# Kernel tuning notes

Hardware: AMD Instinct MI355X
Metric: run time of the kernel (lower is better)

Reference implementation:

```python
import jax, jax.numpy as jnp
import numpy as np

NEG_INF = jnp.finfo(jnp.float32).min


def setup_inputs() -> dict:
    key = jax.random.key(0)
    k1, k2, k3, k4 = jax.random.split(key, 4)
    B, T, C, H = 8, 2048, 1024, 128
    x = jax.random.normal(k1, (B, T, C), dtype=jnp.float32)
    # nn.Linear(n_embd, head_size, bias=False) -> weight [head_size, n_embd]
    s = 1.0 / np.sqrt(C)
    Wk = jax.random.normal(k2, (H, C), dtype=jnp.float32) * s
    Wq = jax.random.normal(k3, (H, C), dtype=jnp.float32) * s
    Wv = jax.random.normal(k4, (H, C), dtype=jnp.float32) * s
    return {"x": x, "Wk": Wk, "Wq": Wq, "Wv": Wv}


def reference(x, Wk, Wq, Wv):
    B, T, C = x.shape
    # projections: x [B,T,C] @ W.T [C,H] -> [B,T,H]
    k = jnp.einsum('btc,hc->bth', x, Wk)
    q = jnp.einsum('btc,hc->bth', x, Wq)
    v = jnp.einsum('btc,hc->bth', x, Wv)
    # NOTE: original scales by C**-0.5 (input channels), faithful here
    scores = jnp.einsum('bqh,bkh->bqk', q, k) * (C ** -0.5)
    causal = jnp.tril(jnp.ones((T, T), dtype=bool))  # tril[:T,:T]
    scores = jnp.where(causal, scores, NEG_INF)
    attn = jax.nn.softmax(scores, axis=-1)
    # dropout(p=0.1) is identity in eval mode; omitted for deterministic reference
    out = jnp.einsum('bqk,bkh->bqh', attn, v)
    return out
```

## Files before the change

### kernel.cpp

```cpp
#include <hip/hip_runtime.h>
#include <hip/hip_bf16.h>

#define B_ 8
#define T_ 2048
#define C_ 1024
#define H_ 128
#define M_ (B_ * T_)

typedef __bf16 bf16x8 __attribute__((ext_vector_type(8)));
typedef __bf16 bf16x4v __attribute__((ext_vector_type(4)));
typedef float f32x4 __attribute__((ext_vector_type(4)));

static __device__ __forceinline__ bf16x8 cvt8(float4 a, float4 b) {
    bf16x8 r;
    r[0] = (__bf16)a.x; r[1] = (__bf16)a.y; r[2] = (__bf16)a.z; r[3] = (__bf16)a.w;
    r[4] = (__bf16)b.x; r[5] = (__bf16)b.y; r[6] = (__bf16)b.z; r[7] = (__bf16)b.w;
    return r;
}


__global__ __launch_bounds__(256) void wprep_kernel(
    const float* __restrict__ Wq, const float* __restrict__ Wk,
    const float* __restrict__ Wv, __bf16* __restrict__ wb)
{
    const int i = blockIdx.x * 256 + threadIdx.x;
    const int w = i >> 15;
    const int jj = i & 32767;
    const float* s = (w == 0) ? Wq : (w == 1) ? Wk : Wv;
    float4 v = ((const float4*)s)[jj];
    bf16x4v o;
    o[0] = (__bf16)v.x; o[1] = (__bf16)v.y; o[2] = (__bf16)v.z; o[3] = (__bf16)v.w;
    *(bf16x4v*)(wb + ((size_t)w << 17) + (size_t)jj * 4) = o;
}

__global__ __launch_bounds__(512) void proj_fused(
    const float* __restrict__ x, const __bf16* __restrict__ wb,
    __bf16* __restrict__ qb, __bf16* __restrict__ kb, __bf16* __restrict__ vTb)
{
    __shared__ __align__(16) __bf16 As[2][64 * 64];
    __shared__ __align__(16) __bf16 Bs[2][384 * 64];

    const int tid = threadIdx.x;
    const int lane = tid & 63;
    const int wid = tid >> 6;
    const int m0 = blockIdx.x * 64;

    const int wr = wid >> 2;
    const int wc = wid & 3;
    const int fr = lane & 15;
    const int g4 = lane >> 4;
    const int rbase = g4 * 4;
    const int sw8 = fr & 7;

    const int arow = tid >> 3;
    const int aslot0 = tid & 7;
    const int aoff = arow * 64 + ((aslot0 ^ (arow & 7)) << 3);
    const float* xrow = x + (size_t)(m0 + arow) * C_ + aslot0 * 8;

    f32x4 acc[2][6];
#pragma unroll
    for (int i = 0; i < 2; i++)
#pragma unroll
        for (int j = 0; j < 6; j++) acc[i][j] = (f32x4){0.f, 0.f, 0.f, 0.f};

    float4 xa = *(const float4*)xrow;
    float4 xb2 = *(const float4*)(xrow + 4);
#pragma unroll
    for (int i = 0; i < 6; i++) {
        const int chunk = i * 512 + tid;
        const int brow = chunk >> 3;
        const int bsrc = ((chunk & 7) ^ (brow & 7)) << 3;
        __builtin_amdgcn_global_load_lds(
            (const __attribute__((address_space(1))) void*)(wb + (size_t)brow * C_ + bsrc),
            (__attribute__((address_space(3))) void*)&Bs[0][chunk * 8], 16, 0, 0);
    }
    *(bf16x8*)&As[0][aoff] = cvt8(xa, xb2);
    __syncthreads();

    for (int kt = 0; kt < 16; kt++) {
        const int cur = kt & 1;

        if (kt < 15) {
            const int k1 = (kt + 1) * 64;
            xa = *(const float4*)(xrow + k1);
            xb2 = *(const float4*)(xrow + k1 + 4);
#pragma unroll
            for (int i = 0; i < 6; i++) {
                const int chunk = i * 512 + tid;
                const int brow = chunk >> 3;
                const int bsrc = ((chunk & 7) ^ (brow & 7)) << 3;
                __builtin_amdgcn_global_load_lds(
                    (const __attribute__((address_space(1))) void*)(wb + (size_t)brow * C_ + k1 + bsrc),
                    (__attribute__((address_space(3))) void*)&Bs[cur ^ 1][chunk * 8], 16, 0, 0);
            }
        }

#pragma unroll
        for (int kk = 0; kk < 2; kk++) {
            const int sc = kk * 4 + g4;
            const int soff = (sc ^ sw8) << 3;
            bf16x8 ar[2], br[6];
#pragma unroll
            for (int i = 0; i < 2; i++)
                ar[i] = *(const bf16x8*)&As[cur][(wr * 32 + i * 16 + fr) * 64 + soff];
#pragma unroll
            for (int j = 0; j < 6; j++)
                br[j] = *(const bf16x8*)&Bs[cur][(wc * 96 + j * 16 + fr) * 64 + soff];
#pragma unroll
            for (int i = 0; i < 2; i++)
#pragma unroll
                for (int j = 0; j < 6; j++)
                    acc[i][j] = __builtin_amdgcn_mfma_f32_16x16x32_bf16(ar[i], br[j], acc[i][j], 0, 0, 0);
        }

        if (kt < 15) {
            *(bf16x8*)&As[cur ^ 1][aoff] = cvt8(xa, xb2);
        }
        __syncthreads();
    }

#pragma unroll
    for (int i = 0; i < 2; i++) {
#pragma unroll
        for (int j = 0; j < 6; j++) {
            const int hg = wc * 96 + j * 16 + fr;
            const int which = hg >> 7;
            const int h = hg & 127;
#pragma unroll
            for (int rr = 0; rr < 4; rr++) {
                const int row = m0 + wr * 32 + i * 16 + rbase + rr;
                const __bf16 val = (__bf16)acc[i][j][rr];
                if (which == 0) {
                    qb[(size_t)row * H_ + h] = val;
                } else if (which == 1) {
                    kb[(size_t)row * H_ + h] = val;
                } else {
                    const int bb = row >> 11;
                    const int tt = row & (T_ - 1);
                    vTb[((size_t)bb * H_ + h) * T_ + tt] = val;
                }
            }
        }
    }
}

__global__ __launch_bounds__(512) void attn_fused(
    const __bf16* __restrict__ qb, const __bf16* __restrict__ kb,
    const __bf16* __restrict__ vTb,
    unsigned int* __restrict__ acc_ws, float* __restrict__ m_ws,
    float* __restrict__ l_ws)
{
    __shared__ __align__(16) __bf16 Klds[2][32 * 128];
    __shared__ __align__(16) __bf16 Vlds[2][128 * 32];
    __shared__ __align__(16) __bf16 pbuf[8][2][16][32];

    const int tid = threadIdx.x;
    const int lane = tid & 63;
    const int wid = tid >> 6;
    const int gw = blockIdx.x;
    const int b = gw & 7;
    const int j = 35 - (gw >> 3);
    int qc = 0;
#pragma unroll
    for (int q = 1; q < 8; q++) qc += (j >= (q * (q + 1)) / 2) ? 1 : 0;
    const int s = j - (qc * (qc + 1)) / 2;
    const int lo = 8 * s, hi = 8 * s + 8;

    const int qrow_loc = qc * 256 + wid * 32;
    const size_t qrow0 = (size_t)b * T_ + qrow_loc;

    const int fr = lane & 15;
    const int g4 = lane >> 4;
    const int koff = g4 * 8;
    const int rbase = g4 * 4;
    const int sw = fr & 6;

    const int krow = tid >> 4, kslot = tid & 15;
    const int vrow = tid >> 2, vslot = tid & 3;
    const __bf16* kgs = kb + ((size_t)b * T_ + krow) * H_ + ((kslot ^ (krow & 15)) << 3);
    const __bf16* vgs = vTb + ((size_t)b * H_ + vrow) * T_ + ((vslot ^ (vrow & 3)) << 3);

    bf16x8 qf[2][4];
#pragma unroll
    for (int g = 0; g < 2; g++) {
        const __bf16* Qb = qb + (qrow0 + g * 16 + fr) * H_ + koff;
#pragma unroll
        for (int hc = 0; hc < 4; hc++)
            qf[g][hc] = *(const bf16x8*)(Qb + hc * 32);
    }

    float m[2] = {-1e30f, -1e30f};
    float l[2] = {0.f, 0.f};
    f32x4 acc[2][8];
#pragma unroll
    for (int g = 0; g < 2; g++)
#pragma unroll
        for (int i = 0; i < 8; i++) acc[g][i] = (f32x4){0.f, 0.f, 0.f, 0.f};

    const float scale = 0.03125f;

    {
        const int k0 = lo * 32, nb = lo & 1;
        __builtin_amdgcn_global_load_lds(
            (const __attribute__((address_space(1))) void*)(kgs + (size_t)k0 * H_),
            (__attribute__((address_space(3))) void*)&Klds[nb][tid * 8], 16, 0, 0);
        __builtin_amdgcn_global_load_lds(
            (const __attribute__((address_space(1))) void*)(vgs + k0),
            (__attribute__((address_space(3))) void*)&Vlds[nb][tid * 8], 16, 0, 0);
    }

    for (int kt = lo; kt < hi; kt++) {
        const int k0 = kt * 32;
        const int pb = kt & 1;

        if (kt + 1 < hi) {
            const int k1 = (kt + 1) * 32, nb = (kt + 1) & 1;
            __builtin_amdgcn_global_load_lds(
                (const __attribute__((address_space(1))) void*)(kgs + (size_t)k1 * H_),
                (__attribute__((address_space(3))) void*)&Klds[nb][tid * 8], 16, 0, 0);
            __builtin_amdgcn_global_load_lds(
                (const __attribute__((address_space(1))) void*)(vgs + k1),
                (__attribute__((address_space(3))) void*)&Vlds[nb][tid * 8], 16, 0, 0);
        }
        __syncthreads();

        if (k0 <= qrow_loc + 31) {
            f32x4 sg[2][2];
#pragma unroll
            for (int g = 0; g < 2; g++) {
                sg[g][0] = (f32x4){0.f, 0.f, 0.f, 0.f};
                sg[g][1] = (f32x4){0.f, 0.f, 0.f, 0.f};
            }
            __builtin_amdgcn_s_setprio(1);
#pragma unroll
            for (int hc = 0; hc < 4; hc++) {
                const int r0 = fr, r1 = 16 + fr;
                bf16x8 kf0 = *(const bf16x8*)&Klds[pb][r0 * 128 + (((hc * 4 + g4) ^ (r0 & 15)) << 3)];
                bf16x8 kf1 = *(const bf16x8*)&Klds[pb][r1 * 128 + (((hc * 4 + g4) ^ (r1 & 15)) << 3)];
#pragma unroll
                for (int g = 0; g < 2; g++) {
                    sg[g][0] = __builtin_amdgcn_mfma_f32_16x16x32_bf16(kf0, qf[g][hc], sg[g][0], 0, 0, 0);
                    sg[g][1] = __builtin_amdgcn_mfma_f32_16x16x32_bf16(kf1, qf[g][hc], sg[g][1], 0, 0, 0);
                }
            }
            __builtin_amdgcn_s_setprio(0);

            float tv[2];
#pragma unroll
            for (int g = 0; g < 2; g++) {
                const int qrow = qrow_loc + g * 16 + fr;
                float t = -1e30f;
#pragma unroll
                for (int h = 0; h < 2; h++) {
#pragma unroll
                    for (int r = 0; r < 4; r++) {
                        const int key = k0 + h * 16 + rbase + r;
                        float v = sg[g][h][r] * scale;
                        v = (key > qrow) ? -1e30f : v;
                        sg[g][h][r] = v;
                        t = fmaxf(t, v);
                    }
                }
                t = fmaxf(t, __shfl_xor(t, 16));
                t = fmaxf(t, __shfl_xor(t, 32));
                tv[g] = t;
            }

            const bool need = (tv[0] > m[0] + 8.0f) || (tv[1] > m[1] + 8.0f);
            if (__any(need)) {
#pragma unroll
                for (int g = 0; g < 2; g++) {
                    const float mnew = fmaxf(m[g], tv[g]);
                    const float corr = __expf(m[g] - mnew);
                    l[g] *= corr;
#pragma unroll
                    for (int r = 0; r < 4; r++) {
                        const float cr = __shfl(corr, rbase + r);
#pragma unroll
                        for (int ht = 0; ht < 8; ht++) acc[g][ht][r] *= cr;
                    }
                    m[g] = mnew;
                }
            }

#pragma unroll
            for (int g = 0; g < 2; g++) {
                bf16x4v p0, p1;
                float sum = 0.f;
#pragma unroll
                for (int r = 0; r < 4; r++) {
                    const float e0 = __expf(sg[g][0][r] - m[g]);
                    const float e1 = __expf(sg[g][1][r] - m[g]);
                    p0[r] = (__bf16)e0;
                    p1[r] = (__bf16)e1;
                    sum += e0 + e1;
                }
                sum += __shfl_xor(sum, 16);
                sum += __shfl_xor(sum, 32);
                l[g] += sum;
                *(bf16x4v*)&pbuf[wid][g][fr][((g4) ^ sw) * 4] = p0;
                *(bf16x4v*)&pbuf[wid][g][fr][((4 + g4) ^ sw) * 4] = p1;
            }

            bf16x8 pa[2];
#pragma unroll
            for (int g = 0; g < 2; g++)
                pa[g] = *(const bf16x8*)&pbuf[wid][g][fr][((2 * g4) ^ sw) * 4];

            __builtin_amdgcn_s_setprio(1);
#pragma unroll
            for (int ht = 0; ht < 8; ht++) {
                const int vr = ht * 16 + fr;
                bf16x8 vf = *(const bf16x8*)&Vlds[pb][vr * 32 + ((g4 ^ (vr & 3)) << 3)];
#pragma unroll
                for (int g = 0; g < 2; g++)
                    acc[g][ht] = __builtin_amdgcn_mfma_f32_16x16x32_bf16(pa[g], vf, acc[g][ht], 0, 0, 0);
            }
            __builtin_amdgcn_s_setprio(0);
        }
        __syncthreads();
    }

#pragma unroll
    for (int g = 0; g < 2; g++) {
        const size_t row0 = qrow0 + g * 16;
#pragma unroll
        for (int p = 0; p < 4; p++) {
#pragma unroll
            for (int r = 0; r < 4; r++) {
                const __bf16 lo2 = (__bf16)acc[g][2 * p][r];
                const __bf16 hi2 = (__bf16)acc[g][2 * p + 1][r];
                const unsigned int w =
                    ((unsigned int)*(const unsigned short*)&hi2 << 16) |
                    *(const unsigned short*)&lo2;
                acc_ws[((size_t)s * M_ + row0 + rbase + r) * 64 + p * 16 + fr] = w;
            }
        }
    }

    if (lane < 16) {
#pragma unroll
        for (int g = 0; g < 2; g++) {
            const size_t row = qrow0 + g * 16 + lane;
            m_ws[(size_t)s * M_ + row] = m[g];
            l_ws[(size_t)s * M_ + row] = l[g];
        }
    }
}

__global__ __launch_bounds__(256) void attn_merge_bal(
    const unsigned int* __restrict__ acc_ws, const float* __restrict__ m_ws,
    const float* __restrict__ l_ws, float* __restrict__ out)
{
    const int lane = threadIdx.x & 63;
    const int g = blockIdx.x * 4 + (threadIdx.x >> 6);
    const int c = 1 + ((g >> 8) & 7);

    float mm = -1e30f;
    for (int s = 0; s < c; s++)
        mm = fmaxf(mm, m_ws[(size_t)s * M_ + g]);
    float ll = 0.f;
    for (int s = 0; s < c; s++)
        ll += l_ws[(size_t)s * M_ + g] * __expf(m_ws[(size_t)s * M_ + g] - mm);
    const float inv = 1.0f / ll;

    float ox = 0.f, oy = 0.f;
    for (int s = 0; s < c; s++) {
        const float sc = __expf(m_ws[(size_t)s * M_ + g] - mm);
        const unsigned int w = acc_ws[((size_t)s * M_ + g) * 64 + lane];
        ox += __uint_as_float((w & 0xffffu) << 16) * sc;
        oy += __uint_as_float(w & 0xffff0000u) * sc;
    }
    ox *= inv; oy *= inv;
    const int col0 = ((lane >> 4) << 5) + (lane & 15);
    out[(size_t)g * H_ + col0] = ox;
    out[(size_t)g * H_ + col0 + 16] = oy;
}

__global__ __launch_bounds__(64) void proj_kernel(
    const float* __restrict__ x,
    const float* __restrict__ Wq, const float* __restrict__ Wk,
    const float* __restrict__ Wv,
    __bf16* __restrict__ qb, __bf16* __restrict__ kb, __bf16* __restrict__ vTb)
{
    const int lane = threadIdx.x;
    const int gw = blockIdx.x;
    const int which = gw >> 10;
    const int mt = gw & 1023;
    const float* W = (which == 0) ? Wq : (which == 1) ? Wk : Wv;
    const int fr = lane & 15;
    const int koff = (lane >> 4) * 8;
    const float* xrow = x + (size_t)(mt * 16 + fr) * C_ + koff;
    const float* wbase = W + (size_t)fr * C_ + koff;
    f32x4 acc[8];
#pragma unroll
    for (int i = 0; i < 8; i++) acc[i] = (f32x4){0.f, 0.f, 0.f, 0.f};
    for (int kc = 0; kc < C_; kc += 32) {
        float4 xa = *(const float4*)(xrow + kc);
        float4 xb2 = *(const float4*)(xrow + kc + 4);
        bf16x8 af = cvt8(xa, xb2);
#pragma unroll
        for (int ht = 0; ht < 8; ht++) {
            const float* wrow = wbase + (size_t)ht * 16 * C_ + kc;
            float4 wa = *(const float4*)(wrow);
            float4 wb2 = *(const float4*)(wrow + 4);
            bf16x8 bfr = cvt8(wa, wb2);
            acc[ht] = __builtin_amdgcn_mfma_f32_16x16x32_bf16(af, bfr, acc[ht], 0, 0, 0);
        }
    }
    const int rbase = (lane >> 4) * 4;
#pragma unroll
    for (int ht = 0; ht < 8; ht++) {
#pragma unroll
        for (int r = 0; r < 4; r++) {
            int row = mt * 16 + rbase + r;
            int h = ht * 16 + fr;
            __bf16 val = (__bf16)acc[ht][r];
            if (which == 0) qb[(size_t)row * H_ + h] = val;
            else if (which == 1) kb[(size_t)row * H_ + h] = val;
            else {
                int bb = row >> 11; int tt = row & (T_ - 1);
                vTb[((size_t)bb * H_ + h) * T_ + tt] = val;
            }
        }
    }
}

__global__ __launch_bounds__(64) void attn_kernel(
    const __bf16* __restrict__ qb, const __bf16* __restrict__ kb,
    const __bf16* __restrict__ vTb, float* __restrict__ out)
{
    __shared__ __align__(16) __bf16 plds[16][32];
    const int lane = threadIdx.x;
    const int gw = blockIdx.x;
    const int b = gw >> 7;
    const int qt = gw & 127;
    const int q0 = qt * 16;
    const int fr = lane & 15;
    const int koff = (lane >> 4) * 8;
    const int rbase = (lane >> 4) * 4;
    const __bf16* Qbase = qb + ((size_t)b * T_ + q0 + fr) * H_ + koff;
    bf16x8 qf[4];
#pragma unroll
    for (int hc = 0; hc < 4; hc++) qf[hc] = *(const bf16x8*)(Qbase + hc * 32);
    float m[4], l[4];
    f32x4 acc[8];
#pragma unroll
    for (int r = 0; r < 4; r++) { m[r] = -1e30f; l[r] = 0.f; }
#pragma unroll
    for (int i = 0; i < 8; i++) acc[i] = (f32x4){0.f, 0.f, 0.f, 0.f};
    const int nkt = (q0 + 15) / 32 + 1;
    const float scale = 0.03125f;
    for (int kt = 0; kt < nkt; kt++) {
        const int k0 = kt * 32;
        f32x4 s0 = (f32x4){0.f, 0.f, 0.f, 0.f};
        f32x4 s1 = (f32x4){0.f, 0.f, 0.f, 0.f};
        const __bf16* Kb0 = kb + ((size_t)b * T_ + k0 + fr) * H_ + koff;
        const __bf16* Kb1 = Kb0 + 16 * H_;
#pragma unroll
        for (int hc = 0; hc < 4; hc++) {
            bf16x8 kf0 = *(const bf16x8*)(Kb0 + hc * 32);
            s0 = __builtin_amdgcn_mfma_f32_16x16x32_bf16(qf[hc], kf0, s0, 0, 0, 0);
            bf16x8 kf1 = *(const bf16x8*)(Kb1 + hc * 32);
            s1 = __builtin_amdgcn_mfma_f32_16x16x32_bf16(qf[hc], kf1, s1, 0, 0, 0);
        }
#pragma unroll
        for (int r = 0; r < 4; r++) {
            const int qrow = q0 + rbase + r;
            float v0 = s0[r] * scale;
            float v1 = s1[r] * scale;
            if (k0 + fr > qrow)      v0 = -1e30f;
            if (k0 + 16 + fr > qrow) v1 = -1e30f;
            float mx = fmaxf(v0, v1);
#pragma unroll
            for (int d = 1; d < 16; d <<= 1) mx = fmaxf(mx, __shfl_xor(mx, d));
            const float mnew = fmaxf(m[r], mx);
            const float corr = __expf(m[r] - mnew);
            const float e0 = __expf(v0 - mnew);
            const float e1 = __expf(v1 - mnew);
            float rs = e0 + e1;
#pragma unroll
            for (int d = 1; d < 16; d <<= 1) rs += __shfl_xor(rs, d);
            l[r] = l[r] * corr + rs;
            m[r] = mnew;
#pragma unroll
            for (int ht = 0; ht < 8; ht++) acc[ht][r] *= corr;
            plds[rbase + r][fr] = (__bf16)e0;
            plds[rbase + r][16 + fr] = (__bf16)e1;
        }
        __syncthreads();
        bf16x8 pa = *(const bf16x8*)(&plds[fr][koff]);
        const __bf16* Vb = vTb + ((size_t)b * H_ + fr) * T_ + k0 + koff;
#pragma unroll
        for (int ht = 0; ht < 8; ht++) {
            bf16x8 vf = *(const bf16x8*)(Vb + (size_t)ht * 16 * T_);
            acc[ht] = __builtin_amdgcn_mfma_f32_16x16x32_bf16(pa, vf, acc[ht], 0, 0, 0);
        }
        __syncthreads();
    }
    float inv[4];
#pragma unroll
    for (int r = 0; r < 4; r++) inv[r] = 1.0f / l[r];
    float* obase = out + ((size_t)b * T_ + q0 + rbase) * H_ + fr;
#pragma unroll
    for (int ht = 0; ht < 8; ht++) {
#pragma unroll
        for (int r = 0; r < 4; r++) {
            obase[(size_t)r * H_ + ht * 16] = acc[ht][r] * inv[r];
        }
    }
}

extern "C" void kernel_launch(void* const* d_in, const int* in_sizes, int n_in,
                              void* d_out, int out_size, void* d_ws, size_t ws_size,
                              hipStream_t stream) {
    const float* x  = (const float*)d_in[0];
    const float* Wk = (const float*)d_in[1];
    const float* Wq = (const float*)d_in[2];
    const float* Wv = (const float*)d_in[3];
    float* out = (float*)d_out;
    uint8_t* ws = (uint8_t*)d_ws;

    const size_t NEED = 47972352;

    if (ws_size >= NEED) {
        unsigned int* acc_ws = (unsigned int*)ws;
        __bf16* wb  = (__bf16*)(ws + 33554432);
        __bf16* qb  = (__bf16*)(ws + 34340864);
        __bf16* kb  = (__bf16*)(ws + 38535168);
        __bf16* vTb = (__bf16*)(ws + 42729472);
        float*  m_ws = (float*)(ws + 46923776);
        float*  l_ws = (float*)(ws + 47448064);

        wprep_kernel<<<384, 256, 0, stream>>>(Wq, Wk, Wv, wb);
        proj_fused<<<M_ / 64, 512, 0, stream>>>(x, wb, qb, kb, vTb);
        attn_fused<<<B_ * 36, 512, 0, stream>>>(qb, kb, vTb, acc_ws, m_ws, l_ws);
        attn_merge_bal<<<M_ / 4, 256, 0, stream>>>(acc_ws, m_ws, l_ws, out);
    } else {
        __bf16* qb  = (__bf16*)d_ws;
        __bf16* kb  = qb + (size_t)M_ * H_;
        __bf16* vTb = kb + (size_t)M_ * H_;
        proj_kernel<<<3072, 64, 0, stream>>>(x, Wq, Wk, Wv, qb, kb, vTb);
        attn_kernel<<<1024, 64, 0, stream>>>(qb, kb, vTb, out);
    }
}
```

Before: 88.63 us.

## Split projection GEMM across N into two 192-column blocks per row tile

The fused QKV projection kernel now splits the 384 output columns into two halves, each handled by a separate 256-thread block. This doubles the grid from 256 to 512 blocks and halves the LDS used for B per block. Block indices are arranged so that the two halves of the same row tile are scheduled near each other, which lets the re-read fp32 x data hit in cache. The intent is better occupancy and load balance across the CUs, at the cost of loading and converting x twice.

```diff
diff --git a/kernel.cpp b/kernel.cpp
--- a/kernel.cpp
+++ b/kernel.cpp
@@ -33,29 +33,41 @@
     *(bf16x4v*)(wb + ((size_t)w << 17) + (size_t)jj * 4) = o;
 }
 
-__global__ __launch_bounds__(512) void proj_fused(
+__global__ __launch_bounds__(256) void proj_fused(
     const float* __restrict__ x, const __bf16* __restrict__ wb,
     __bf16* __restrict__ qb, __bf16* __restrict__ kb, __bf16* __restrict__ vTb)
 {
     __shared__ __align__(16) __bf16 As[2][64 * 64];
-    __shared__ __align__(16) __bf16 Bs[2][384 * 64];
+    __shared__ __align__(16) __bf16 Bs[2][192 * 64];
 
     const int tid = threadIdx.x;
     const int lane = tid & 63;
     const int wid = tid >> 6;
-    const int m0 = blockIdx.x * 64;
-
-    const int wr = wid >> 2;
-    const int wc = wid & 3;
+    const int bx = blockIdx.x;
+    const int base16 = bx >> 4;
+    const int rem16 = bx & 15;
+    const int which2 = rem16 >> 3;
+    const int mt = base16 * 8 + (rem16 & 7);
+    const int m0 = mt * 64;
+    const int n0 = which2 * 192;
+
+    const int wr = wid >> 1;
+    const int wc = wid & 1;
     const int fr = lane & 15;
     const int g4 = lane >> 4;
     const int rbase = g4 * 4;
     const int sw8 = fr & 7;
 
-    const int arow = tid >> 3;
-    const int aslot0 = tid & 7;
-    const int aoff = arow * 64 + ((aslot0 ^ (arow & 7)) << 3);
-    const float* xrow = x + (size_t)(m0 + arow) * C_ + aslot0 * 8;
+    int aoff[2];
+    const float* xrow[2];
+#pragma unroll
+    for (int c = 0; c < 2; c++) {
+        const int chunk = c * 256 + tid;
+        const int arow = chunk >> 3;
+        const int aslot = chunk & 7;
+        aoff[c] = arow * 64 + ((aslot ^ (arow & 7)) << 3);
+        xrow[c] = x + (size_t)(m0 + arow) * C_ + aslot * 8;
+    }
 
     f32x4 acc[2][6];
 #pragma unroll
@@ -63,18 +75,24 @@
 #pragma unroll
         for (int j = 0; j < 6; j++) acc[i][j] = (f32x4){0.f, 0.f, 0.f, 0.f};
 
-    float4 xa = *(const float4*)xrow;
-    float4 xb2 = *(const float4*)(xrow + 4);
+    float4 xa[2], xb2[2];
+#pragma unroll
+    for (int c = 0; c < 2; c++) {
+        xa[c] = *(const float4*)xrow[c];
+        xb2[c] = *(const float4*)(xrow[c] + 4);
+    }
 #pragma unroll
     for (int i = 0; i < 6; i++) {
-        const int chunk = i * 512 + tid;
+        const int chunk = i * 256 + tid;
         const int brow = chunk >> 3;
         const int bsrc = ((chunk & 7) ^ (brow & 7)) << 3;
         __builtin_amdgcn_global_load_lds(
-            (const __attribute__((address_space(1))) void*)(wb + (size_t)brow * C_ + bsrc),
+            (const __attribute__((address_space(1))) void*)(wb + (size_t)(n0 + brow) * C_ + bsrc),
             (__attribute__((address_space(3))) void*)&Bs[0][chunk * 8], 16, 0, 0);
     }
-    *(bf16x8*)&As[0][aoff] = cvt8(xa, xb2);
+#pragma unroll
+    for (int c = 0; c < 2; c++)
+        *(bf16x8*)&As[0][aoff[c]] = cvt8(xa[c], xb2[c]);
     __syncthreads();
 
     for (int kt = 0; kt < 16; kt++) {
@@ -82,15 +100,18 @@
 
         if (kt < 15) {
             const int k1 = (kt + 1) * 64;
-            xa = *(const float4*)(xrow + k1);
-            xb2 = *(const float4*)(xrow + k1 + 4);
+#pragma unroll
+            for (int c = 0; c < 2; c++) {
+                xa[c] = *(const float4*)(xrow[c] + k1);
+                xb2[c] = *(const float4*)(xrow[c] + k1 + 4);
+            }
 #pragma unroll
             for (int i = 0; i < 6; i++) {
-                const int chunk = i * 512 + tid;
+                const int chunk = i * 256 + tid;
                 const int brow = chunk >> 3;
                 const int bsrc = ((chunk & 7) ^ (brow & 7)) << 3;
                 __builtin_amdgcn_global_load_lds(
-                    (const __attribute__((address_space(1))) void*)(wb + (size_t)brow * C_ + k1 + bsrc),
+                    (const __attribute__((address_space(1))) void*)(wb + (size_t)(n0 + brow) * C_ + k1 + bsrc),
                     (__attribute__((address_space(3))) void*)&Bs[cur ^ 1][chunk * 8], 16, 0, 0);
             }
         }
@@ -114,7 +135,9 @@
         }
 
         if (kt < 15) {
-            *(bf16x8*)&As[cur ^ 1][aoff] = cvt8(xa, xb2);
+#pragma unroll
+            for (int c = 0; c < 2; c++)
+                *(bf16x8*)&As[cur ^ 1][aoff[c]] = cvt8(xa[c], xb2[c]);
         }
         __syncthreads();
     }
@@ -123,7 +146,7 @@
     for (int i = 0; i < 2; i++) {
 #pragma unroll
         for (int j = 0; j < 6; j++) {
-            const int hg = wc * 96 + j * 16 + fr;
+            const int hg = n0 + wc * 96 + j * 16 + fr;
             const int which = hg >> 7;
             const int h = hg & 127;
 #pragma unroll
@@ -533,7 +556,7 @@
         float*  l_ws = (float*)(ws + 47448064);
 
         wprep_kernel<<<384, 256, 0, stream>>>(Wq, Wk, Wv, wb);
-        proj_fused<<<M_ / 64, 512, 0, stream>>>(x, wb, qb, kb, vTb);
+        proj_fused<<<512, 256, 0, stream>>>(x, wb, qb, kb, vTb);
         attn_fused<<<B_ * 36, 512, 0, stream>>>(qb, kb, vTb, acc_ws, m_ws, l_ws);
         attn_merge_bal<<<M_ / 4, 256, 0, stream>>>(acc_ws, m_ws, l_ws, out);
     } else {
```

Result: slower. 94.69 us (+6.8%).
